# Performance work log

Measured on AMD Instinct MI355X. Metric: run time of the kernel, lower is better.

The kernel has to match this reference:

```python
import jax, jax.numpy as jnp
import numpy as np

EPS_COS = 1e-8
EPS_SHARP = 1e-16


def setup_inputs() -> dict:
    key = jax.random.key(0)
    k1, k2, k3, k4 = jax.random.split(key, 4)
    B, H, R, C, M = 512, 512, 2048, 64, 3
    out_dim = 3 * C + 2 * M + 4  # 202
    h = jax.random.normal(k1, (B, H), dtype=jnp.float32)
    prev_w = jax.random.uniform(k2, (B, R), dtype=jnp.float32)
    prev_w = prev_w / prev_w.sum(axis=1, keepdims=True)  # valid focus distribution
    memory = jax.random.normal(k3, (B, R, C), dtype=jnp.float32)
    fc_w = jax.random.normal(k4, (out_dim, H), dtype=jnp.float32) * 0.05
    fc_b = jnp.zeros((out_dim,), dtype=jnp.float32)
    return {"h": h, "prev_w": prev_w, "memory": memory, "fc_w": fc_w, "fc_b": fc_b}


def _write_head(h, prev_w, memory, fc_w, fc_b):
    B, R, C = memory.shape
    total = fc_w.shape[0]
    shift_len = total - 3 * C - 3          # 2*max_shift + 1
    m = (shift_len - 1) // 2               # max_shift

    z = h @ fc_w.T + fc_b                  # [B, total]
    sizes = [C, 1, 1, shift_len, 1, C, C]
    offs = np.cumsum([0] + sizes)
    k     = jnp.tanh(z[:, offs[0]:offs[1]])                 # [B, C]
    beta  = jax.nn.softplus(z[:, offs[1]:offs[2]])          # [B, 1]
    g     = jax.nn.sigmoid(z[:, offs[2]:offs[3]])           # [B, 1]
    s     = jax.nn.softmax(z[:, offs[3]:offs[4]], axis=1)   # [B, 2m+1]
    gamma = jax.nn.softplus(z[:, offs[4]:offs[5]]) + 1.0    # [B, 1]
    e     = jax.nn.sigmoid(z[:, offs[5]:offs[6]])           # [B, C]
    a     = jnp.tanh(z[:, offs[6]:offs[7]])                 # [B, C]

    # content addressing: cosine similarity of k vs each memory row
    num = jnp.einsum('bc,brc->br', k, memory)
    k_n = jnp.maximum(jnp.linalg.norm(k, axis=1, keepdims=True), EPS_COS)   # [B,1]
    m_n = jnp.maximum(jnp.linalg.norm(memory, axis=2), EPS_COS)             # [B,R]
    w_c = jax.nn.softmax(beta * (num / (k_n * m_n)), axis=1)                # [B,R]

    # gated interpolation
    w_g = g * w_c + (1.0 - g) * prev_w                                      # [B,R]

    # circular shift (per-sample cross-correlation, O(B*R*(2m+1)))
    unrolled = jnp.concatenate([w_g[:, -m:], w_g, w_g[:, :m]], axis=1)      # [B, R+2m]
    windows = jnp.stack([unrolled[:, j:j + R] for j in range(2 * m + 1)], axis=1)  # [B,2m+1,R]
    w_s = jnp.einsum('bjr,bj->br', windows, s)                              # [B,R]

    # sharpen
    w_p = jnp.power(w_s, gamma)
    w = w_p / (w_p.sum(axis=1, keepdims=True) + EPS_SHARP)                  # [B,R]

    # erase + write (fused)
    wE = w[:, :, None]                                                      # [B,R,1]
    new_mem = memory * (1.0 - wE * e[:, None, :]) + wE * a[:, None, :]      # [B,R,C]
    return w, new_mem


def reference(h, prev_w, memory, fc_w, fc_b):
    return _write_head(h, prev_w, memory, fc_w, fc_b)
```

## Files before the change

kernel.cpp:

```cpp
#include <hip/hip_runtime.h>
#include <math.h>

#define BB 512
#define HH 512
#define RR 2048
#define CC 64
#define OUTD 202
#define PSTRIDE 208
#define K_OFF 0
#define E_OFF 64
#define A_OFF 128
#define S_OFF 192
#define COMBO_OFF 199
#define G_OFF 200
#define GAMMA_OFF 201

typedef float f32x4 __attribute__((ext_vector_type(4)));

__device__ __forceinline__ float softplusf_(float x) {
    return (x > 20.f) ? x : log1pf(expf(x));
}
__device__ __forceinline__ float sigmoidf_(float x) {
    return 1.f / (1.f + expf(-x));
}

__global__ __launch_bounds__(256) void params_kernel(
    const float* __restrict__ h, const float* __restrict__ fc_w,
    const float* __restrict__ fc_b, float* __restrict__ pw)
{
    __shared__ float h_sh[8][HH];
    __shared__ float z_sh[8][204];
    const int tid = threadIdx.x;
    const int b0 = blockIdx.x * 8;

    for (int idx = tid; idx < 8 * HH; idx += 256) {
        int j = idx >> 9, i = idx & 511;
        h_sh[j][i] = h[(size_t)(b0 + j) * HH + i];
    }
    __syncthreads();

    if (tid < OUTD) {
        float acc[8];
        #pragma unroll
        for (int j = 0; j < 8; ++j) acc[j] = 0.f;
        const float4* wr4 = (const float4*)(fc_w + (size_t)tid * HH);
        for (int i4 = 0; i4 < HH / 4; ++i4) {
            float4 wv = wr4[i4];
            int i = i4 * 4;
            #pragma unroll
            for (int j = 0; j < 8; ++j) {
                acc[j] = fmaf(wv.x, h_sh[j][i + 0], acc[j]);
                acc[j] = fmaf(wv.y, h_sh[j][i + 1], acc[j]);
                acc[j] = fmaf(wv.z, h_sh[j][i + 2], acc[j]);
                acc[j] = fmaf(wv.w, h_sh[j][i + 3], acc[j]);
            }
        }
        float bias = fc_b[tid];
        #pragma unroll
        for (int j = 0; j < 8; ++j) z_sh[j][tid] = acc[j] + bias;
    }
    __syncthreads();

    for (int idx = tid; idx < 8 * OUTD; idx += 256) {
        int j = idx / OUTD;
        int t = idx - j * OUTD;
        float z = z_sh[j][t];
        float* p = pw + (size_t)(b0 + j) * PSTRIDE;
        if (t < 64)            p[K_OFF + t] = tanhf(z);
        else if (t == 65)      p[G_OFF] = sigmoidf_(z);
        else if (t == 73)      p[GAMMA_OFF] = softplusf_(z) + 1.f;
        else if (t >= 74 && t < 138) p[E_OFF + (t - 74)] = sigmoidf_(z);
        else if (t >= 138)     p[A_OFF + (t - 138)] = tanhf(z);
    }
    __syncthreads();

    if (tid < 8) {
        int j = tid;
        float* p = pw + (size_t)(b0 + j) * PSTRIDE;
        float ss = 0.f;
        for (int c = 0; c < 64; ++c) {
            float kv = tanhf(z_sh[j][c]);
            ss += kv * kv;
        }
        float kn = fmaxf(sqrtf(ss), 1e-8f);
        float beta = softplusf_(z_sh[j][64]);
        p[COMBO_OFF] = beta / kn;
        float mx = -1e30f;
        for (int q = 0; q < 7; ++q) mx = fmaxf(mx, z_sh[j][66 + q]);
        float ev[7], se = 0.f;
        for (int q = 0; q < 7; ++q) { ev[q] = expf(z_sh[j][66 + q] - mx); se += ev[q]; }
        float inv = 1.f / se;
        for (int q = 0; q < 7; ++q) p[S_OFF + q] = ev[q] * inv;
    }
}

__global__ __launch_bounds__(256) void score_kernel(
    const float* __restrict__ memory, const float* __restrict__ pw,
    float* __restrict__ sc)
{
    const int tid = threadIdx.x;
    const int b = blockIdx.x >> 2;
    const int rbase = (blockIdx.x & 3) * 512;
    const int lane16 = tid & 15;
    const int rgrp = tid >> 4;
    const float* p = pw + (size_t)b * PSTRIDE;
    const float4 k4 = *(const float4*)(p + K_OFF + lane16 * 4);
    const float combo = p[COMBO_OFF];
    const float* memb = memory + (size_t)b * RR * CC;

    #pragma unroll 8
    for (int i = 0; i < 32; ++i) {
        int r = rbase + i * 16 + rgrp;
        float4 m4 = *(const float4*)(memb + (size_t)r * CC + lane16 * 4);
        float num = m4.x * k4.x + m4.y * k4.y + m4.z * k4.z + m4.w * k4.w;
        float ssq = m4.x * m4.x + m4.y * m4.y + m4.z * m4.z + m4.w * m4.w;
        #pragma unroll
        for (int m = 1; m < 16; m <<= 1) {
            num += __shfl_xor(num, m, 64);
            ssq += __shfl_xor(ssq, m, 64);
        }
        if (lane16 == 0) {
            float mn = fmaxf(sqrtf(ssq), 1e-8f);
            sc[(size_t)b * RR + r] = __expf(combo * num / mn);
        }
    }
}

__device__ __forceinline__ float block_reduce_sum256(float v, float* red) {
    #pragma unroll
    for (int m = 1; m < 64; m <<= 1) v += __shfl_xor(v, m, 64);
    int wid = threadIdx.x >> 6;
    if ((threadIdx.x & 63) == 0) red[wid] = v;
    __syncthreads();
    float x = red[0] + red[1] + red[2] + red[3];
    __syncthreads();
    return x;
}

__global__ __launch_bounds__(256) void weight_kernel(
    const float* __restrict__ sc, const float* __restrict__ prev_w,
    const float* __restrict__ pw, float* __restrict__ out_w)
{
    __shared__ float buf[RR];
    __shared__ float wg[RR];
    __shared__ float red[4];
    const int b = blockIdx.x;
    const int tid = threadIdx.x;
    const float* p = pw + (size_t)b * PSTRIDE;
    const float g = p[G_OFF];
    const float gamma = p[GAMMA_OFF];
    const float s0 = p[S_OFF + 0], s1 = p[S_OFF + 1], s2 = p[S_OFF + 2],
                s3 = p[S_OFF + 3], s4 = p[S_OFF + 4], s5 = p[S_OFF + 5],
                s6 = p[S_OFF + 6];

    float ls = 0.f;
    for (int r = tid; r < RR; r += 256) {
        float ev = sc[(size_t)b * RR + r];
        buf[r] = ev;
        ls += ev;
    }
    const float se = block_reduce_sum256(ls, red);
    const float invse = 1.f / se;

    for (int r = tid; r < RR; r += 256) {
        wg[r] = g * (buf[r] * invse) + (1.f - g) * prev_w[(size_t)b * RR + r];
    }
    __syncthreads();

    float lp = 0.f;
    for (int r = tid; r < RR; r += 256) {
        float acc = s0 * wg[(r - 3) & (RR - 1)]
                  + s1 * wg[(r - 2) & (RR - 1)]
                  + s2 * wg[(r - 1) & (RR - 1)]
                  + s3 * wg[r]
                  + s4 * wg[(r + 1) & (RR - 1)]
                  + s5 * wg[(r + 2) & (RR - 1)]
                  + s6 * wg[(r + 3) & (RR - 1)];
        float wp = __powf(acc, gamma);
        buf[r] = wp;
        lp += wp;
    }
    const float ps = block_reduce_sum256(lp, red);
    const float invp = 1.f / (ps + 1e-16f);

    for (int r = tid; r < RR; r += 256) {
        out_w[(size_t)b * RR + r] = buf[r] * invp;
    }
}

__global__ __launch_bounds__(256) void update_kernel(
    const float* __restrict__ memory, const float* __restrict__ w,
    const float* __restrict__ pw, float* __restrict__ out_mem)
{
    const int bid = (int)gridDim.x - 1 - (int)blockIdx.x;
    const int b = bid >> 2;
    const int rbase = (bid & 3) * 512;
    const int tid = threadIdx.x;
    const int lane16 = tid & 15;
    const int rgrp = tid >> 4;
    const float* p = pw + (size_t)b * PSTRIDE;
    const f32x4 e4 = *(const f32x4*)(p + E_OFF + lane16 * 4);
    const f32x4 a4 = *(const f32x4*)(p + A_OFF + lane16 * 4);
    const float* memb = memory + (size_t)b * RR * CC;
    float* omb = out_mem + (size_t)b * RR * CC;
    const float* wb = w + (size_t)b * RR;

    #pragma unroll 8
    for (int i = 0; i < 32; ++i) {
        int r = rbase + i * 16 + rgrp;
        float wv = wb[r];
        const f32x4* mp = (const f32x4*)(memb + (size_t)r * CC) + lane16;
        f32x4 m4 = __builtin_nontemporal_load(mp);
        f32x4 o;
        o.x = m4.x * (1.f - wv * e4.x) + wv * a4.x;
        o.y = m4.y * (1.f - wv * e4.y) + wv * a4.y;
        o.z = m4.z * (1.f - wv * e4.z) + wv * a4.z;
        o.w = m4.w * (1.f - wv * e4.w) + wv * a4.w;
        __builtin_nontemporal_store(o, (f32x4*)(omb + (size_t)r * CC) + lane16);
    }
}

extern "C" void kernel_launch(void* const* d_in, const int* in_sizes, int n_in,
                              void* d_out, int out_size, void* d_ws, size_t ws_size,
                              hipStream_t stream) {
    const float* h      = (const float*)d_in[0];
    const float* prev_w = (const float*)d_in[1];
    const float* memory = (const float*)d_in[2];
    const float* fc_w   = (const float*)d_in[3];
    const float* fc_b   = (const float*)d_in[4];

    float* pw      = (float*)d_ws;
    float* out_w   = (float*)d_out;
    float* out_mem = out_w + (size_t)BB * RR;
    float* sc      = out_mem;

    params_kernel<<<64, 256, 0, stream>>>(h, fc_w, fc_b, pw);
    score_kernel<<<BB * 4, 256, 0, stream>>>(memory, pw, sc);
    weight_kernel<<<BB, 256, 0, stream>>>(sc, prev_w, pw, out_w);
    update_kernel<<<BB * 4, 256, 0, stream>>>(memory, out_w, pw, out_mem);
}
```

Before: 199.1 us.

## Fuse score, weighting and memory update into one per-batch kernel

```diff
diff --git a/kernel.cpp b/kernel.cpp
--- a/kernel.cpp
+++ b/kernel.cpp
@@ -94,129 +94,140 @@
     }
 }
 
-__global__ __launch_bounds__(256) void score_kernel(
-    const float* __restrict__ memory, const float* __restrict__ pw,
-    float* __restrict__ sc)
-{
-    const int tid = threadIdx.x;
-    const int b = blockIdx.x >> 2;
-    const int rbase = (blockIdx.x & 3) * 512;
-    const int lane16 = tid & 15;
-    const int rgrp = tid >> 4;
-    const float* p = pw + (size_t)b * PSTRIDE;
-    const float4 k4 = *(const float4*)(p + K_OFF + lane16 * 4);
-    const float combo = p[COMBO_OFF];
-    const float* memb = memory + (size_t)b * RR * CC;
-
-    #pragma unroll 8
-    for (int i = 0; i < 32; ++i) {
-        int r = rbase + i * 16 + rgrp;
-        float4 m4 = *(const float4*)(memb + (size_t)r * CC + lane16 * 4);
-        float num = m4.x * k4.x + m4.y * k4.y + m4.z * k4.z + m4.w * k4.w;
-        float ssq = m4.x * m4.x + m4.y * m4.y + m4.z * m4.z + m4.w * m4.w;
-        #pragma unroll
-        for (int m = 1; m < 16; m <<= 1) {
-            num += __shfl_xor(num, m, 64);
-            ssq += __shfl_xor(ssq, m, 64);
-        }
-        if (lane16 == 0) {
-            float mn = fmaxf(sqrtf(ssq), 1e-8f);
-            sc[(size_t)b * RR + r] = __expf(combo * num / mn);
-        }
-    }
-}
-
-__device__ __forceinline__ float block_reduce_sum256(float v, float* red) {
+__device__ __forceinline__ float block_reduce_sum16(float v, float* red) {
     #pragma unroll
     for (int m = 1; m < 64; m <<= 1) v += __shfl_xor(v, m, 64);
     int wid = threadIdx.x >> 6;
     if ((threadIdx.x & 63) == 0) red[wid] = v;
     __syncthreads();
-    float x = red[0] + red[1] + red[2] + red[3];
-    __syncthreads();
-    return x;
-}
-
-__global__ __launch_bounds__(256) void weight_kernel(
-    const float* __restrict__ sc, const float* __restrict__ prev_w,
-    const float* __restrict__ pw, float* __restrict__ out_w)
+    if (threadIdx.x < 16) {
+        float x = red[threadIdx.x];
+        #pragma unroll
+        for (int m = 1; m < 16; m <<= 1) x += __shfl_xor(x, m, 64);
+        if (threadIdx.x == 0) red[0] = x;
+    }
+    __syncthreads();
+    float r = red[0];
+    __syncthreads();
+    return r;
+}
+
+__global__ __launch_bounds__(1024) void fused_kernel(
+    const float* __restrict__ memory, const float* __restrict__ prev_w,
+    const float* __restrict__ pw, float* __restrict__ out_w,
+    float* __restrict__ out_mem)
 {
-    __shared__ float buf[RR];
+    __shared__ float evs[RR];
     __shared__ float wg[RR];
-    __shared__ float red[4];
+    __shared__ float red[16];
+
     const int b = blockIdx.x;
     const int tid = threadIdx.x;
+    const int lane8 = tid & 7;
+    const int rgrp = tid >> 3;
     const float* p = pw + (size_t)b * PSTRIDE;
+
+    const f32x4 ka = *(const f32x4*)(p + K_OFF + lane8 * 8);
+    const f32x4 kb = *(const f32x4*)(p + K_OFF + lane8 * 8 + 4);
+    const float combo = p[COMBO_OFF];
+    const float* memb = memory + (size_t)b * RR * CC;
+
+    float lsum = 0.f;
+    #pragma unroll 8
+    for (int i = 0; i < 16; ++i) {
+        int r = i * 128 + rgrp;
+        const f32x4* mp = (const f32x4*)(memb + (size_t)r * CC + lane8 * 8);
+        f32x4 ma = mp[0];
+        f32x4 mb = mp[1];
+        float num = ma.x * ka.x + ma.y * ka.y + ma.z * ka.z + ma.w * ka.w
+                  + mb.x * kb.x + mb.y * kb.y + mb.z * kb.z + mb.w * kb.w;
+        float ssq = ma.x * ma.x + ma.y * ma.y + ma.z * ma.z + ma.w * ma.w
+                  + mb.x * mb.x + mb.y * mb.y + mb.z * mb.z + mb.w * mb.w;
+        #pragma unroll
+        for (int m = 1; m < 8; m <<= 1) {
+            num += __shfl_xor(num, m, 64);
+            ssq += __shfl_xor(ssq, m, 64);
+        }
+        if (lane8 == 0) {
+            float mn = fmaxf(sqrtf(ssq), 1e-8f);
+            float ev = __expf(combo * num / mn);
+            evs[r] = ev;
+            lsum += ev;
+        }
+    }
+    const float se = block_reduce_sum16(lsum, red);
+
     const float g = p[G_OFF];
     const float gamma = p[GAMMA_OFF];
     const float s0 = p[S_OFF + 0], s1 = p[S_OFF + 1], s2 = p[S_OFF + 2],
                 s3 = p[S_OFF + 3], s4 = p[S_OFF + 4], s5 = p[S_OFF + 5],
                 s6 = p[S_OFF + 6];
-
-    float ls = 0.f;
-    for (int r = tid; r < RR; r += 256) {
-        float ev = sc[(size_t)b * RR + r];
-        buf[r] = ev;
-        ls += ev;
-    }
-    const float se = block_reduce_sum256(ls, red);
-    const float invse = 1.f / se;
-
-    for (int r = tid; r < RR; r += 256) {
-        wg[r] = g * (buf[r] * invse) + (1.f - g) * prev_w[(size_t)b * RR + r];
+    const float gi = g / se, omg = 1.f - g;
+
+    {
+        const int r2 = tid * 2;
+        float2 pv = *(const float2*)(prev_w + (size_t)b * RR + r2);
+        wg[r2]     = gi * evs[r2]     + omg * pv.x;
+        wg[r2 + 1] = gi * evs[r2 + 1] + omg * pv.y;
     }
     __syncthreads();
 
     float lp = 0.f;
-    for (int r = tid; r < RR; r += 256) {
-        float acc = s0 * wg[(r - 3) & (RR - 1)]
-                  + s1 * wg[(r - 2) & (RR - 1)]
-                  + s2 * wg[(r - 1) & (RR - 1)]
-                  + s3 * wg[r]
-                  + s4 * wg[(r + 1) & (RR - 1)]
-                  + s5 * wg[(r + 2) & (RR - 1)]
-                  + s6 * wg[(r + 3) & (RR - 1)];
-        float wp = __powf(acc, gamma);
-        buf[r] = wp;
-        lp += wp;
-    }
-    const float ps = block_reduce_sum256(lp, red);
+    {
+        const int r2 = tid * 2;
+        #pragma unroll
+        for (int q = 0; q < 2; ++q) {
+            int r = r2 + q;
+            float acc = s0 * wg[(r - 3) & (RR - 1)]
+                      + s1 * wg[(r - 2) & (RR - 1)]
+                      + s2 * wg[(r - 1) & (RR - 1)]
+                      + s3 * wg[r]
+                      + s4 * wg[(r + 1) & (RR - 1)]
+                      + s5 * wg[(r + 2) & (RR - 1)]
+                      + s6 * wg[(r + 3) & (RR - 1)];
+            float v = __powf(acc, gamma);
+            evs[r] = v;
+            lp += v;
+        }
+    }
+    const float ps = block_reduce_sum16(lp, red);
     const float invp = 1.f / (ps + 1e-16f);
 
-    for (int r = tid; r < RR; r += 256) {
-        out_w[(size_t)b * RR + r] = buf[r] * invp;
-    }
-}
-
-__global__ __launch_bounds__(256) void update_kernel(
-    const float* __restrict__ memory, const float* __restrict__ w,
-    const float* __restrict__ pw, float* __restrict__ out_mem)
-{
-    const int bid = (int)gridDim.x - 1 - (int)blockIdx.x;
-    const int b = bid >> 2;
-    const int rbase = (bid & 3) * 512;
-    const int tid = threadIdx.x;
-    const int lane16 = tid & 15;
-    const int rgrp = tid >> 4;
-    const float* p = pw + (size_t)b * PSTRIDE;
-    const f32x4 e4 = *(const f32x4*)(p + E_OFF + lane16 * 4);
-    const f32x4 a4 = *(const f32x4*)(p + A_OFF + lane16 * 4);
-    const float* memb = memory + (size_t)b * RR * CC;
+    {
+        const int r2 = tid * 2;
+        float w0 = evs[r2] * invp;
+        float w1 = evs[r2 + 1] * invp;
+        wg[r2] = w0;
+        wg[r2 + 1] = w1;
+        *(float2*)(out_w + (size_t)b * RR + r2) = make_float2(w0, w1);
+    }
+    __syncthreads();
+
+    const f32x4 ea = *(const f32x4*)(p + E_OFF + lane8 * 8);
+    const f32x4 eb = *(const f32x4*)(p + E_OFF + lane8 * 8 + 4);
+    const f32x4 aa = *(const f32x4*)(p + A_OFF + lane8 * 8);
+    const f32x4 ab = *(const f32x4*)(p + A_OFF + lane8 * 8 + 4);
     float* omb = out_mem + (size_t)b * RR * CC;
-    const float* wb = w + (size_t)b * RR;
 
     #pragma unroll 8
-    for (int i = 0; i < 32; ++i) {
-        int r = rbase + i * 16 + rgrp;
-        float wv = wb[r];
-        const f32x4* mp = (const f32x4*)(memb + (size_t)r * CC) + lane16;
-        f32x4 m4 = __builtin_nontemporal_load(mp);
-        f32x4 o;
-        o.x = m4.x * (1.f - wv * e4.x) + wv * a4.x;
-        o.y = m4.y * (1.f - wv * e4.y) + wv * a4.y;
-        o.z = m4.z * (1.f - wv * e4.z) + wv * a4.z;
-        o.w = m4.w * (1.f - wv * e4.w) + wv * a4.w;
-        __builtin_nontemporal_store(o, (f32x4*)(omb + (size_t)r * CC) + lane16);
+    for (int i = 0; i < 16; ++i) {
+        int r = i * 128 + rgrp;
+        float wv = wg[r];
+        const f32x4* mp = (const f32x4*)(memb + (size_t)r * CC + lane8 * 8);
+        f32x4 ma = mp[0];
+        f32x4 mb = mp[1];
+        f32x4 oa, ob;
+        oa.x = ma.x * (1.f - wv * ea.x) + wv * aa.x;
+        oa.y = ma.y * (1.f - wv * ea.y) + wv * aa.y;
+        oa.z = ma.z * (1.f - wv * ea.z) + wv * aa.z;
+        oa.w = ma.w * (1.f - wv * ea.w) + wv * aa.w;
+        ob.x = mb.x * (1.f - wv * eb.x) + wv * ab.x;
+        ob.y = mb.y * (1.f - wv * eb.y) + wv * ab.y;
+        ob.z = mb.z * (1.f - wv * eb.z) + wv * ab.z;
+        ob.w = mb.w * (1.f - wv * eb.w) + wv * ab.w;
+        f32x4* op = (f32x4*)(omb + (size_t)r * CC + lane8 * 8);
+        __builtin_nontemporal_store(oa, op);
+        __builtin_nontemporal_store(ob, op + 1);
     }
 }
 
@@ -232,10 +243,7 @@
     float* pw      = (float*)d_ws;
     float* out_w   = (float*)d_out;
     float* out_mem = out_w + (size_t)BB * RR;
-    float* sc      = out_mem;
 
     params_kernel<<<64, 256, 0, stream>>>(h, fc_w, fc_b, pw);
-    score_kernel<<<BB * 4, 256, 0, stream>>>(memory, pw, sc);
-    weight_kernel<<<BB, 256, 0, stream>>>(sc, prev_w, pw, out_w);
-    update_kernel<<<BB * 4, 256, 0, stream>>>(memory, out_w, pw, out_mem);
-}
+    fused_kernel<<<BB, 1024, 0, stream>>>(memory, prev_w, pw, out_w, out_mem);
+}
```

New measurement: 220.5 us. +10.7%, slower.
